# Kernel tuning notes

Hardware: AMD Instinct MI355X
Metric: run time of the kernel (lower is better)

## Reference

```python
import jax, jax.numpy as jnp
import numpy as np

B, S, D = 4, 2048, 1024
H, A = 16, 64


def setup_inputs() -> dict:
    key = jax.random.key(0)
    ks = jax.random.split(key, 9)
    return {
        "q": jax.random.normal(ks[0], (B, S, D), dtype=jnp.float32),
        "k": jax.random.normal(ks[1], (B, S, D), dtype=jnp.float32),
        "v": jax.random.normal(ks[2], (B, S, D), dtype=jnp.float32),
        "Wq": jax.random.normal(ks[3], (H, D, A), dtype=jnp.float32) * (1.0 / np.sqrt(D)),
        "bq": jax.random.normal(ks[4], (H, A), dtype=jnp.float32) * 0.01,
        "Wk": jax.random.normal(ks[5], (H, D, A), dtype=jnp.float32) * (1.0 / np.sqrt(D)),
        "bk": jax.random.normal(ks[6], (H, A), dtype=jnp.float32) * 0.01,
        "Wv": jax.random.normal(ks[7], (H, D, A), dtype=jnp.float32) * (1.0 / np.sqrt(D)),
        "bv": jax.random.normal(ks[8], (H, A), dtype=jnp.float32) * 0.01,
    }


def reference(q, k, v, Wq, bq, Wk, bk, Wv, bv):
    # Per-head linear projections (batched over heads): [B,H,S,A]
    qh = jnp.einsum("bsd,hda->bhsa", q, Wq) + bq[None, :, None, :]
    kh = jnp.einsum("bsd,hda->bhsa", k, Wk) + bk[None, :, None, :]
    vh = jnp.einsum("bsd,hda->bhsa", v, Wv) + bv[None, :, None, :]
    # NOTE: original has NO 1/sqrt(d) scaling and no mask.
    scores = jnp.einsum("bhqa,bhka->bhqk", qh, kh)  # [B,H,S,S]
    weights = jax.nn.softmax(scores, axis=-1)
    attn = jnp.einsum("bhqk,bhka->bhqa", weights, vh)  # [B,H,S,A]
    # concat heads on last dim: [B,S,H*A]
    return jnp.transpose(attn, (0, 2, 1, 3)).reshape(q.shape[0], q.shape[1], -1)
```

## Files before the change

kernel.cpp:

```cpp
#include <hip/hip_runtime.h>
#include <stdint.h>

#define B_ 4
#define S_ 2048
#define D_ 1024
#define H_ 16
#define A_ 64
#define M_ (B_*S_)
#define BH_ (B_*H_)
#define INV_LN2 1.4426950408889634f

typedef _Float16 f16x8 __attribute__((ext_vector_type(8)));
typedef float    f32x4 __attribute__((ext_vector_type(4)));

__device__ __forceinline__ uint32_t f2h(float f) {
    _Float16 h = (_Float16)f;
    return (uint32_t)__builtin_bit_cast(uint16_t, h);
}

__device__ __forceinline__ float exp2f_fast(float x) {
    return __builtin_amdgcn_exp2f(x);
}

__device__ __forceinline__ uint32_t pkrtz(float a, float b) {
    return __builtin_bit_cast(uint32_t, __builtin_amdgcn_cvt_pkrtz(a, b));
}

__device__ __forceinline__ int swz(int row, int col) {
    return (row * 64 + col) ^ ((row & 7) << 3);
}

__global__ __launch_bounds__(256) void prep_w(
    const float* __restrict__ Wq, const float* __restrict__ Wk, const float* __restrict__ Wv,
    uint16_t* __restrict__ Wt)
{
    __shared__ float tile[64][65];
    const int dt = blockIdx.x, h = blockIdx.y, p = blockIdx.z;
    const float* W = (p == 0) ? Wq : (p == 1) ? Wk : Wv;
    const float sc = (p == 0) ? INV_LN2 : 1.0f;
    const float* src = W + (h * D_ + dt * 64) * A_;
    const int t = threadIdx.x;
    const int r0 = t >> 4, c4 = (t & 15) * 4;
    #pragma unroll
    for (int i = 0; i < 4; i++) {
        int r = r0 + i * 16;
        float4 x = *(const float4*)(src + r * A_ + c4);
        tile[r][c4] = x.x; tile[r][c4 + 1] = x.y; tile[r][c4 + 2] = x.z; tile[r][c4 + 3] = x.w;
    }
    __syncthreads();
    uint16_t* dst = Wt + (p * H_ + h) * (A_ * D_) + dt * 64;
    #pragma unroll
    for (int i = 0; i < 4; i++) {
        int a = r0 + i * 16;
        int d4 = (t & 15) * 4;
        uint2 o2;
        o2.x = f2h(tile[d4][a] * sc)     | (f2h(tile[d4 + 1][a] * sc) << 16);
        o2.y = f2h(tile[d4 + 2][a] * sc) | (f2h(tile[d4 + 3][a] * sc) << 16);
        *(uint2*)(dst + a * D_ + d4) = o2;
    }
}

__global__ __launch_bounds__(512) void proj_kernel(
    const float* __restrict__ qsrc, const float* __restrict__ ksrc, const float* __restrict__ vsrc,
    const uint16_t* __restrict__ Wt,
    const float* __restrict__ bq, const float* __restrict__ bk, const float* __restrict__ bv,
    uint16_t* __restrict__ qh, uint16_t* __restrict__ kh, uint16_t* __restrict__ vpv)
{
    __shared__ __align__(16) float    Asf[128 * 32];
    __shared__ __align__(16) uint16_t Bs[256 * 32];
    const int p = blockIdx.z, nt = blockIdx.y, mt = blockIdx.x;
    const int t = threadIdx.x, lane = t & 63, w = t >> 6;
    const int wr = w >> 2, wc = w & 3;
    const int lr = lane & 15, lg = lane >> 4;
    const int Mbase = mt * 128;
    const float* Af = (p == 0) ? qsrc : (p == 1) ? ksrc : vsrc;

    const int ar = t >> 3;
    const int asl = (t & 7) ^ (ar & 7);
    const float* asrc = Af + (size_t)(Mbase + ar) * D_ + asl * 4;

    const int br = t >> 2;
    const int bsl = (t & 3) ^ ((br >> 1) & 3);
    const uint16_t* bsrc[2];
    #pragma unroll
    for (int i = 0; i < 2; i++) {
        int row = br + 128 * i;
        bsrc[i] = Wt + ((size_t)(p * H_ + nt * 4 + (row >> 6)) * A_ + (row & 63)) * D_ + bsl * 8;
    }

    f32x4 acc[4][4] = {};

    for (int kk = 0; kk < D_; kk += 32) {
        __builtin_amdgcn_global_load_lds(asrc + kk,                  (char*)Asf + w * 1024,        16, 0, 0);
        __builtin_amdgcn_global_load_lds(asrc + kk + (size_t)64 * D_,(char*)Asf + 8192 + w * 1024, 16, 0, 0);
        __builtin_amdgcn_global_load_lds(bsrc[0] + kk, (char*)Bs + w * 1024,        16, 0, 0);
        __builtin_amdgcn_global_load_lds(bsrc[1] + kk, (char*)Bs + 8192 + w * 1024, 16, 0, 0);
        __syncthreads();

        f16x8 af[4], bf[4];
        #pragma unroll
        for (int mb = 0; mb < 4; mb++) {
            const int r = wr * 64 + mb * 16 + lr;
            const int c = r & 7;
            const float* base = Asf + r * 32;
            f32x4 lo = *(const f32x4*)(base + (((2 * lg)     ^ c) << 2));
            f32x4 hi = *(const f32x4*)(base + (((2 * lg + 1) ^ c) << 2));
            uint4 u;
            u.x = pkrtz(lo[0], lo[1]); u.y = pkrtz(lo[2], lo[3]);
            u.z = pkrtz(hi[0], hi[1]); u.w = pkrtz(hi[2], hi[3]);
            af[mb] = __builtin_bit_cast(f16x8, u);
        }
        #pragma unroll
        for (int nb = 0; nb < 4; nb++) {
            const int r = wc * 64 + nb * 16 + lr;
            const int ph = lg ^ ((r >> 1) & 3);
            bf[nb] = *(const f16x8*)(Bs + r * 32 + ph * 8);
        }
        #pragma unroll
        for (int mb = 0; mb < 4; mb++) {
            #pragma unroll
            for (int nb = 0; nb < 4; nb++)
                acc[mb][nb] = __builtin_amdgcn_mfma_f32_16x16x32_f16(af[mb], bf[nb], acc[mb][nb], 0, 0, 0);
        }
        __syncthreads();
    }

    const int h = nt * 4 + wc;
    const int b = Mbase >> 11;
    const int bh = b * H_ + h;
    const int sbase = Mbase & (S_ - 1);
    const float* bias = ((p == 0) ? bq : (p == 1) ? bk : bv) + h * A_;
    const float bsc = (p == 0) ? INV_LN2 : 1.0f;
    #pragma unroll
    for (int mb = 0; mb < 4; mb++) {
        #pragma unroll
        for (int nb = 0; nb < 4; nb++) {
            const int a = nb * 16 + lr;
            const float bia = bias[a] * bsc;
            const int s0 = sbase + wr * 64 + mb * 16 + 4 * lg;
            if (p < 2) {
                uint16_t* o = (p == 0) ? qh : kh;
                #pragma unroll
                for (int r = 0; r < 4; r++)
                    o[(bh * S_ + s0 + r) * A_ + a] = (uint16_t)f2h(acc[mb][nb][r] + bia);
            } else {
                const int kt2 = s0 >> 6, kv0 = s0 & 63;
                const int kb2 = kv0 >> 5, jhi = (kv0 >> 4) & 1, lg2 = (kv0 >> 2) & 3;
                uint2 pk2;
                pk2.x = f2h(acc[mb][nb][0] + bia) | (f2h(acc[mb][nb][1] + bia) << 16);
                pk2.y = f2h(acc[mb][nb][2] + bia) | (f2h(acc[mb][nb][3] + bia) << 16);
                *(uint2*)(vpv + ((size_t)((bh * 32 + kt2) * 512 + kb2 * 256 + lg2 * 64 + a)) * 8 + 4 * jhi) = pk2;
            }
        }
    }
}

__global__ __launch_bounds__(512, 8) void flash_kernel(
    const uint16_t* __restrict__ qh, const uint16_t* __restrict__ kh,
    const uint16_t* __restrict__ vpv, float* __restrict__ out)
{
    __shared__ __align__(16) uint16_t smem[16384];
    const int t = threadIdx.x, lane = t & 63, w = t >> 6;
    const int lr = lane & 15, lg = lane >> 4;

    const int flat = blockIdx.y * gridDim.x + blockIdx.x;
    const int nf = (flat & 7) * 128 + (flat >> 3);
    const int qt = nf & 15, bh = nf >> 4;
    const int b = bh >> 4, h = bh & (H_ - 1);

    f16x8 qf[2];
    {
        const uint16_t* qp = qh + (size_t)(bh * S_ + qt * 128 + w * 16 + lr) * A_ + 8 * lg;
        qf[0] = *(const f16x8*)(qp);
        qf[1] = *(const f16x8*)(qp + 32);
    }
    f16x8 ones;
    #pragma unroll
    for (int j = 0; j < 8; j++) ones[j] = (_Float16)1.0f;

    const int row0 = t >> 3;
    const int col0 = (t * 8) & 63;
    const int scol = col0 ^ ((row0 & 7) << 3);
    const uint16_t* kg = kh + (size_t)(bh * S_ + row0) * A_ + scol;
    const uint16_t* vg = vpv + (size_t)bh * (S_ * A_) + t * 8;

    f32x4 negm = {};
    f32x4 oacc[4] = {};
    f32x4 lsum = {};

    #define STAGE(buf, kt_) do {                                                          \
        __builtin_amdgcn_global_load_lds(kg + (size_t)(kt_) * (64 * A_),                  \
                                         smem + (buf) * 4096 + w * 512, 16, 0, 0);        \
        __builtin_amdgcn_global_load_lds(vg + (size_t)(kt_) * 4096,                       \
                                         smem + 8192 + (buf) * 4096 + w * 512, 16, 0, 0); \
    } while (0)

    const int NT = S_ / 64;
    STAGE(0, 0);
    __syncthreads();

    for (int kt = 0; kt < NT; kt++) {
        const int cur = kt & 1;
        if (kt + 1 < NT) STAGE(cur ^ 1, kt + 1);
        const uint16_t* Kc = smem + cur * 4096;
        const uint16_t* Vc = smem + 8192 + cur * 4096;

        f32x4 sacc[4];
        __builtin_amdgcn_s_setprio(1);
        #pragma unroll
        for (int nb = 0; nb < 4; nb++) {
            f16x8 kf = *(const f16x8*)(Kc + swz(nb * 16 + lr, 8 * lg));
            sacc[nb] = __builtin_amdgcn_mfma_f32_16x16x32_f16(kf, qf[0], negm, 0, 0, 0);
        }
        #pragma unroll
        for (int nb = 0; nb < 4; nb++) {
            f16x8 kf = *(const f16x8*)(Kc + swz(nb * 16 + lr, 32 + 8 * lg));
            sacc[nb] = __builtin_amdgcn_mfma_f32_16x16x32_f16(kf, qf[1], sacc[nb], 0, 0, 0);
        }
        __builtin_amdgcn_s_setprio(0);

        float a0 = fmaxf(fmaxf(sacc[0][0], sacc[0][1]), sacc[0][2]);
        float a1 = fmaxf(fmaxf(sacc[0][3], sacc[1][0]), sacc[1][1]);
        float a2 = fmaxf(fmaxf(sacc[1][2], sacc[1][3]), sacc[2][0]);
        float a3 = fmaxf(fmaxf(sacc[2][1], sacc[2][2]), sacc[2][3]);
        float a4 = fmaxf(fmaxf(sacc[3][0], sacc[3][1]), sacc[3][2]);
        float pm = fmaxf(fmaxf(fmaxf(a0, a1), fmaxf(a2, a3)), fmaxf(a4, sacc[3][3]));

        if (__any(pm > 11.0f)) {
            float tm = fmaxf(pm, __shfl_xor(pm, 16));
            tm = fmaxf(tm, __shfl_xor(tm, 32));
            float delta = fmaxf(tm, 0.0f);
            float sc = exp2f_fast(-delta);
            #pragma unroll
            for (int r = 0; r < 4; r++) negm[r] -= delta;
            #pragma unroll
            for (int nb = 0; nb < 4; nb++) {
                #pragma unroll
                for (int r = 0; r < 4; r++) sacc[nb][r] -= delta;
            }
            float scr[4];
            #pragma unroll
            for (int r = 0; r < 4; r++) scr[r] = __shfl(sc, 4 * lg + r);
            #pragma unroll
            for (int r = 0; r < 4; r++) lsum[r] *= scr[r];
            #pragma unroll
            for (int nb = 0; nb < 4; nb++) {
                #pragma unroll
                for (int r = 0; r < 4; r++) oacc[nb][r] *= scr[r];
            }
        }

        f16x8 paf[2];
        #pragma unroll
        for (int kb2 = 0; kb2 < 2; kb2++) {
            float e[8];
            #pragma unroll
            for (int jh = 0; jh < 2; jh++) {
                #pragma unroll
                for (int r = 0; r < 4; r++)
                    e[jh * 4 + r] = exp2f_fast(sacc[2 * kb2 + jh][r]);
            }
            uint4 u;
            u.x = pkrtz(e[0], e[1]); u.y = pkrtz(e[2], e[3]);
            u.z = pkrtz(e[4], e[5]); u.w = pkrtz(e[6], e[7]);
            paf[kb2] = __builtin_bit_cast(f16x8, u);
        }

        __builtin_amdgcn_s_setprio(1);
        lsum = __builtin_amdgcn_mfma_f32_16x16x32_f16(paf[0], ones, lsum, 0, 0, 0);
        lsum = __builtin_amdgcn_mfma_f32_16x16x32_f16(paf[1], ones, lsum, 0, 0, 0);
        #pragma unroll
        for (int kb2 = 0; kb2 < 2; kb2++) {
            #pragma unroll
            for (int nb = 0; nb < 4; nb++) {
                f16x8 vf = *(const f16x8*)(Vc + ((kb2 * 4 + lg) * 64 + nb * 16 + lr) * 8);
                oacc[nb] = __builtin_amdgcn_mfma_f32_16x16x32_f16(paf[kb2], vf, oacc[nb], 0, 0, 0);
            }
        }
        __builtin_amdgcn_s_setprio(0);
        __syncthreads();
    }
    #undef STAGE

    float* outs = (float*)smem;
    #pragma unroll
    for (int r = 0; r < 4; r++) {
        const float inv = 1.0f / lsum[r];
        const int sl = w * 16 + 4 * lg + r;
        #pragma unroll
        for (int nb = 0; nb < 4; nb++)
            outs[sl * 64 + nb * 16 + lr] = oacc[nb][r] * inv;
    }
    __syncthreads();
    const int orow = t >> 4, oslot = t & 15;
    float* obase = out + (size_t)(b * S_ + qt * 128 + orow) * (H_ * A_) + h * A_ + oslot * 4;
    #pragma unroll
    for (int i = 0; i < 4; i++)
        *(float4*)(obase + (size_t)(32 * i) * (H_ * A_)) =
            *(const float4*)(outs + (orow + 32 * i) * 64 + oslot * 4);
}

extern "C" void kernel_launch(void* const* d_in, const int* in_sizes, int n_in,
                              void* d_out, int out_size, void* d_ws, size_t ws_size,
                              hipStream_t stream)
{
    const float* q  = (const float*)d_in[0];
    const float* k  = (const float*)d_in[1];
    const float* v  = (const float*)d_in[2];
    const float* Wq = (const float*)d_in[3];
    const float* bq = (const float*)d_in[4];
    const float* Wk = (const float*)d_in[5];
    const float* bk = (const float*)d_in[6];
    const float* Wv = (const float*)d_in[7];
    const float* bv = (const float*)d_in[8];
    float* out = (float*)d_out;

    uint8_t* ws = (uint8_t*)d_ws;
    const size_t SZ_H  = (size_t)BH_ * S_ * A_ * 2;
    uint16_t* qh  = (uint16_t*)(ws);
    uint16_t* kh  = (uint16_t*)(ws + SZ_H);
    uint16_t* vpv = (uint16_t*)(ws + 2 * SZ_H);
    uint16_t* Wt  = (uint16_t*)(ws + 3 * SZ_H);

    prep_w<<<dim3(16, H_, 3), 256, 0, stream>>>(Wq, Wk, Wv, Wt);
    proj_kernel<<<dim3(M_ / 128, 4, 3), 512, 0, stream>>>(q, k, v, Wt,
                                                          bq, bk, bv, qh, kh, vpv);
    flash_kernel<<<dim3(S_ / 128, BH_), 512, 0, stream>>>(qh, kh, vpv, out);
}
```

Before: 191.8 us.

## Double-buffer projection GEMM and triple-buffer flash attention K/V staging

The projection GEMM now double-buffers its A and B LDS tiles. It prefetches the next k-slice with global_load_lds before computing the current one, and uses explicit vmcnt waits and raw barriers in place of full __syncthreads. The flash kernel moves from two to three K/V LDS buffers, issuing loads two tiles ahead so there is one barrier per iteration. The aim is to hide global-memory latency behind MFMA work and cut synchronisation stalls. The cost is more LDS per block (projection 32KB to 64KB, flash 32KB to 48KB), which can lower how many blocks fit on each CU.

```diff
diff --git a/kernel.cpp b/kernel.cpp
--- a/kernel.cpp
+++ b/kernel.cpp
@@ -66,8 +66,8 @@
     const float* __restrict__ bq, const float* __restrict__ bk, const float* __restrict__ bv,
     uint16_t* __restrict__ qh, uint16_t* __restrict__ kh, uint16_t* __restrict__ vpv)
 {
-    __shared__ __align__(16) float    Asf[128 * 32];
-    __shared__ __align__(16) uint16_t Bs[256 * 32];
+    __shared__ __align__(16) float    Asf[2][128 * 32];
+    __shared__ __align__(16) uint16_t Bs[2][256 * 32];
     const int p = blockIdx.z, nt = blockIdx.y, mt = blockIdx.x;
     const int t = threadIdx.x, lane = t & 63, w = t >> 6;
     const int wr = w >> 2, wc = w & 3;
@@ -90,19 +90,37 @@
 
     f32x4 acc[4][4] = {};
 
-    for (int kk = 0; kk < D_; kk += 32) {
-        __builtin_amdgcn_global_load_lds(asrc + kk,                  (char*)Asf + w * 1024,        16, 0, 0);
-        __builtin_amdgcn_global_load_lds(asrc + kk + (size_t)64 * D_,(char*)Asf + 8192 + w * 1024, 16, 0, 0);
-        __builtin_amdgcn_global_load_lds(bsrc[0] + kk, (char*)Bs + w * 1024,        16, 0, 0);
-        __builtin_amdgcn_global_load_lds(bsrc[1] + kk, (char*)Bs + 8192 + w * 1024, 16, 0, 0);
-        __syncthreads();
+    #define PSTAGE(buf, kkv) do {                                                                  \
+        __builtin_amdgcn_global_load_lds(asrc + (kkv),                                             \
+                                         (char*)(&Asf[buf][0]) + w * 1024,        16, 0, 0);       \
+        __builtin_amdgcn_global_load_lds(asrc + (kkv) + (size_t)64 * D_,                           \
+                                         (char*)(&Asf[buf][0]) + 8192 + w * 1024, 16, 0, 0);       \
+        __builtin_amdgcn_global_load_lds(bsrc[0] + (kkv),                                          \
+                                         (char*)(&Bs[buf][0]) + w * 1024,         16, 0, 0);       \
+        __builtin_amdgcn_global_load_lds(bsrc[1] + (kkv),                                          \
+                                         (char*)(&Bs[buf][0]) + 8192 + w * 1024,  16, 0, 0);       \
+    } while (0)
+
+    const int NKS = D_ / 32;
+    PSTAGE(0, 0);
+
+    for (int ks = 0; ks < NKS; ks++) {
+        const int cur = ks & 1;
+        if (ks + 1 < NKS) {
+            PSTAGE(cur ^ 1, (ks + 1) * 32);
+            asm volatile("s_waitcnt vmcnt(4)" ::: "memory");
+        } else {
+            asm volatile("s_waitcnt vmcnt(0)" ::: "memory");
+        }
+        __builtin_amdgcn_s_barrier();
+        __builtin_amdgcn_sched_barrier(0);
 
         f16x8 af[4], bf[4];
         #pragma unroll
         for (int mb = 0; mb < 4; mb++) {
             const int r = wr * 64 + mb * 16 + lr;
             const int c = r & 7;
-            const float* base = Asf + r * 32;
+            const float* base = &Asf[cur][0] + r * 32;
             f32x4 lo = *(const f32x4*)(base + (((2 * lg)     ^ c) << 2));
             f32x4 hi = *(const f32x4*)(base + (((2 * lg + 1) ^ c) << 2));
             uint4 u;
@@ -114,7 +132,7 @@
         for (int nb = 0; nb < 4; nb++) {
             const int r = wc * 64 + nb * 16 + lr;
             const int ph = lg ^ ((r >> 1) & 3);
-            bf[nb] = *(const f16x8*)(Bs + r * 32 + ph * 8);
+            bf[nb] = *(const f16x8*)(&Bs[cur][0] + r * 32 + ph * 8);
         }
         #pragma unroll
         for (int mb = 0; mb < 4; mb++) {
@@ -122,8 +140,10 @@
             for (int nb = 0; nb < 4; nb++)
                 acc[mb][nb] = __builtin_amdgcn_mfma_f32_16x16x32_f16(af[mb], bf[nb], acc[mb][nb], 0, 0, 0);
         }
-        __syncthreads();
-    }
+        __builtin_amdgcn_s_barrier();
+        __builtin_amdgcn_sched_barrier(0);
+    }
+    #undef PSTAGE
 
     const int h = nt * 4 + wc;
     const int b = Mbase >> 11;
@@ -159,7 +179,7 @@
     const uint16_t* __restrict__ qh, const uint16_t* __restrict__ kh,
     const uint16_t* __restrict__ vpv, float* __restrict__ out)
 {
-    __shared__ __align__(16) uint16_t smem[16384];
+    __shared__ __align__(16) uint16_t smem[24576];
     const int t = threadIdx.x, lane = t & 63, w = t >> 6;
     const int lr = lane & 15, lg = lane >> 4;
 
@@ -188,22 +208,30 @@
     f32x4 oacc[4] = {};
     f32x4 lsum = {};
 
-    #define STAGE(buf, kt_) do {                                                          \
+    #define FSTAGE(buf, kt_) do {                                                         \
         __builtin_amdgcn_global_load_lds(kg + (size_t)(kt_) * (64 * A_),                  \
                                          smem + (buf) * 4096 + w * 512, 16, 0, 0);        \
         __builtin_amdgcn_global_load_lds(vg + (size_t)(kt_) * 4096,                       \
-                                         smem + 8192 + (buf) * 4096 + w * 512, 16, 0, 0); \
+                                         smem + 12288 + (buf) * 4096 + w * 512, 16, 0, 0);\
     } while (0)
 
     const int NT = S_ / 64;
-    STAGE(0, 0);
-    __syncthreads();
-
+    FSTAGE(0, 0);
+    FSTAGE(1, 1);
+
+    int cur = 0;
     for (int kt = 0; kt < NT; kt++) {
-        const int cur = kt & 1;
-        if (kt + 1 < NT) STAGE(cur ^ 1, kt + 1);
+        if (kt < NT - 1) asm volatile("s_waitcnt vmcnt(2)" ::: "memory");
+        else             asm volatile("s_waitcnt vmcnt(0)" ::: "memory");
+        __builtin_amdgcn_s_barrier();
+        __builtin_amdgcn_sched_barrier(0);
+        if (kt + 2 < NT) {
+            int nb2 = cur + 2; if (nb2 >= 3) nb2 -= 3;
+            FSTAGE(nb2, kt + 2);
+        }
+        __builtin_amdgcn_sched_barrier(0);
         const uint16_t* Kc = smem + cur * 4096;
-        const uint16_t* Vc = smem + 8192 + cur * 4096;
+        const uint16_t* Vc = smem + 12288 + cur * 4096;
 
         f32x4 sacc[4];
         __builtin_amdgcn_s_setprio(1);
@@ -278,10 +306,12 @@
             }
         }
         __builtin_amdgcn_s_setprio(0);
-        __syncthreads();
-    }
-    #undef STAGE
-
+
+        cur = (cur == 2) ? 0 : cur + 1;
+    }
+    #undef FSTAGE
+
+    __syncthreads();
     float* outs = (float*)smem;
     #pragma unroll
     for (int r = 0; r < 4; r++) {
```

After: 170.6 us. 1.12x faster.
